# Kernel tuning notes

Measured on AMD Instinct MI355X. Metric: run time of the kernel, lower is better.

The kernel has to match this reference:

```python
import jax, jax.numpy as jnp
import numpy as np

N_NODES = 16384
N_EDGES = 196608
N_ELEM = 8
C = 32              # hidden channels per l-block
LMAX = 3
SH_DIM = 16         # (LMAX+1)^2
NUM_BESSEL = 8
R_MAX = 5.0
P_CUT = 5.0
H_RAD = 64
AVG_NEIGH = 12.0
N_LAYERS = 2
L_SLICES = ((0, 1), (1, 4), (4, 9), (9, 16))  # l = 0..3 blocks


def real_sph_harm(u):
    # u: [E,3] unit vectors -> real spherical harmonics up to l=3, component-normalized. [E,16]
    x, y, z = u[:, 0], u[:, 1], u[:, 2]
    x2, y2, z2 = x * x, y * y, z * z
    sh = [
        jnp.ones_like(x),
        jnp.sqrt(3.) * x, jnp.sqrt(3.) * y, jnp.sqrt(3.) * z,
        jnp.sqrt(15.) * x * y, jnp.sqrt(15.) * y * z,
        jnp.sqrt(5.) / 2. * (3. * z2 - 1.), jnp.sqrt(15.) * x * z,
        jnp.sqrt(15.) / 2. * (x2 - y2),
        jnp.sqrt(35. / 8.) * y * (3. * x2 - y2), jnp.sqrt(105.) * x * y * z,
        jnp.sqrt(21. / 8.) * y * (5. * z2 - 1.), jnp.sqrt(7.) / 2. * z * (5. * z2 - 3.),
        jnp.sqrt(21. / 8.) * x * (5. * z2 - 1.), jnp.sqrt(105.) / 2. * z * (x2 - y2),
        jnp.sqrt(35. / 8.) * x * (x2 - 3. * y2),
    ]
    return jnp.stack(sh, axis=-1)


def bessel_cutoff(r):
    # Bessel radial basis * polynomial cutoff (MACE radial embedding). r: [E] -> [E, NUM_BESSEL]
    u = r / R_MAX
    n = jnp.arange(1, NUM_BESSEL + 1, dtype=r.dtype)
    safe_r = jnp.maximum(r, 1e-9)
    rb = jnp.sqrt(2.0 / R_MAX) * jnp.sin(jnp.pi * n * u[:, None]) / safe_r[:, None]
    p = P_CUT
    fc = 1.0 - (p + 1.) * (p + 2.) / 2. * u ** p + p * (p + 2.) * u ** (p + 1.) - p * (p + 1.) / 2. * u ** (p + 2.)
    fc = fc * (u < 1.0).astype(r.dtype)
    return rb * fc[:, None]


def per_l_linear(a, W):
    # equivariant per-l channel mixing. a: [N,C,16], W: [4,C,C]
    outs = [jnp.einsum('nci,co->noi', a[:, :, s:e], W[l]) for l, (s, e) in enumerate(L_SLICES)]
    return jnp.concatenate(outs, axis=-1)


def mace_descriptors(atom_pos, node_attrs, shifts, edge_index,
                     W_embed, W1, W2, W3, W4, Wlin, Wskip, w2, w3, Wprod):
    snd, rcv = edge_index[0], edge_index[1]
    vec = atom_pos[rcv] - atom_pos[snd] + shifts            # [E,3]
    length = jnp.sqrt(jnp.sum(vec * vec, axis=-1) + 1e-18)  # [E]
    unit = vec / length[:, None]
    edge_attrs = real_sph_harm(unit)                        # [E,16]
    edge_feats = bessel_cutoff(length)                      # [E,8]

    node_scal = node_attrs @ W_embed                        # [N,C] node embedding (l=0)
    node_feats = jnp.zeros((atom_pos.shape[0], C, SH_DIM), dtype=atom_pos.dtype).at[:, :, 0].set(node_scal)

    descs = []
    for i in range(N_LAYERS):
        # radial MLP -> per-edge tensor-product weights
        h = jax.nn.silu(edge_feats @ W1[i])
        h = jax.nn.silu(h @ W2[i])
        h = jax.nn.silu(h @ W3[i])
        tpw = (h @ W4[i]).reshape(-1, C, SH_DIM)            # [E,C,16]
        # gather -> channelwise tensor product with edge spherical harmonics
        s = node_feats[:, :, 0][snd]                        # [E,C] invariant sender feats
        msg = tpw * edge_attrs[:, None, :] * s[:, :, None]  # [E,C,16]
        # scatter-add aggregation
        agg = jax.ops.segment_sum(msg.reshape(-1, C * SH_DIM), rcv,
                                  num_segments=N_NODES) / AVG_NEIGH
        a = per_l_linear(agg.reshape(-1, C, SH_DIM), Wlin[i])
        # element-dependent residual (skip tensor product with one-hot node attrs)
        sc = jnp.einsum('nz,ncm,zco->nom', node_attrs, node_feats, Wskip[i])
        # symmetric-contraction-style product block (correlation up to 3, invariants)
        inv = a[:, :, 0]
        p2 = jnp.sum(a * a, axis=-1)                        # power-spectrum invariant [N,C]
        b0 = inv + w2[i] * p2 + w3[i] * inv * p2
        b = a.at[:, :, 0].set(b0)
        node_feats = per_l_linear(b, Wprod[i]) + sc
        descs.append(node_feats[:, :, 0])                   # invariant slice
    return jnp.concatenate(descs, axis=-1)                  # [N, N_LAYERS*C]


def setup_inputs() -> dict:
    key = jax.random.key(0)
    ks = jax.random.split(key, 16)
    atom_pos = jax.random.normal(ks[0], (N_NODES, 3), dtype=jnp.float32) * 1.8
    elem = jax.random.randint(ks[1], (N_NODES,), 0, N_ELEM)
    node_attrs = jax.nn.one_hot(elem, N_ELEM, dtype=jnp.float32)
    shifts = jnp.zeros((N_EDGES, 3), dtype=jnp.float32)
    edge_index = jax.random.randint(ks[2], (2, N_EDGES), 0, N_NODES)
    f32 = jnp.float32
    W_embed = jax.random.normal(ks[3], (N_ELEM, C), f32) / np.sqrt(N_ELEM)
    W1 = jax.random.normal(ks[4], (N_LAYERS, NUM_BESSEL, H_RAD), f32) / np.sqrt(NUM_BESSEL)
    W2 = jax.random.normal(ks[5], (N_LAYERS, H_RAD, H_RAD), f32) / np.sqrt(H_RAD)
    W3 = jax.random.normal(ks[6], (N_LAYERS, H_RAD, H_RAD), f32) / np.sqrt(H_RAD)
    W4 = jax.random.normal(ks[7], (N_LAYERS, H_RAD, C * SH_DIM), f32) / np.sqrt(H_RAD)
    Wlin = jax.random.normal(ks[8], (N_LAYERS, 4, C, C), f32) / np.sqrt(C)
    Wskip = jax.random.normal(ks[9], (N_LAYERS, N_ELEM, C, C), f32) / np.sqrt(N_ELEM * C)
    w2 = jax.random.normal(ks[10], (N_LAYERS, C), f32) * 0.1
    w3 = jax.random.normal(ks[11], (N_LAYERS, C), f32) * 0.1
    Wprod = jax.random.normal(ks[12], (N_LAYERS, 4, C, C), f32) / np.sqrt(C)
    return {"atom_pos": atom_pos, "node_attrs": node_attrs, "shifts": shifts,
            "edge_index": edge_index, "W_embed": W_embed, "W1": W1, "W2": W2,
            "W3": W3, "W4": W4, "Wlin": Wlin, "Wskip": Wskip, "w2": w2,
            "w3": w3, "Wprod": Wprod}


def reference(atom_pos, node_attrs, shifts, edge_index, W_embed, W1, W2, W3, W4,
              Wlin, Wskip, w2, w3, Wprod):
    return mace_descriptors(atom_pos, node_attrs, shifts, edge_index,
                            W_embed, W1, W2, W3, W4, Wlin, Wskip, w2, w3, Wprod)
```

## Files before the change

### kernel.cpp

```cpp
#include <hip/hip_runtime.h>
#include <math.h>

#define N_NODES_C 16384
#define N_EDGES_C 196608

typedef short bf16x8 __attribute__((ext_vector_type(8)));
typedef float f32x4 __attribute__((ext_vector_type(4)));
typedef float f32x8 __attribute__((ext_vector_type(8)));

__device__ __forceinline__ float silu_f(float x) {
  return x * __builtin_amdgcn_rcpf(1.0f + __expf(-x));
}

__global__ void k_count(const int* __restrict__ rcv, int* __restrict__ counts) {
  int e = blockIdx.x * 256 + threadIdx.x;
  atomicAdd(&counts[rcv[e]], 1);
}

__global__ __launch_bounds__(1024) void k_scan(const int* __restrict__ counts,
                                               int* __restrict__ row_start,
                                               int* __restrict__ cursor) {
  __shared__ int sums[1024];
  const int tid = threadIdx.x;
  int loc[16];
  int s = 0;
#pragma unroll
  for (int i = 0; i < 16; ++i) { loc[i] = counts[tid * 16 + i]; s += loc[i]; }
  sums[tid] = s;
  __syncthreads();
  for (int off = 1; off < 1024; off <<= 1) {
    int t = (tid >= off) ? sums[tid - off] : 0;
    __syncthreads();
    sums[tid] += t;
    __syncthreads();
  }
  int excl = sums[tid] - s;
#pragma unroll
  for (int i = 0; i < 16; ++i) {
    row_start[tid * 16 + i] = excl;
    cursor[tid * 16 + i] = excl;
    excl += loc[i];
  }
  if (tid == 1023) row_start[N_NODES_C] = excl;
}

__global__ void k_fill(const int* __restrict__ rcv, int* __restrict__ cursor,
                       int* __restrict__ elist) {
  int e = blockIdx.x * 256 + threadIdx.x;
  int slot = atomicAdd(&cursor[rcv[e]], 1);
  elist[slot] = e;
}

__global__ void k_elem(const float* __restrict__ attrs, int* __restrict__ elem) {
  int n = blockIdx.x * 256 + threadIdx.x;
  const float* a = attrs + n * 8;
  int best = 0;
  float bv = a[0];
#pragma unroll
  for (int z = 1; z < 8; ++z) {
    if (a[z] > bv) { bv = a[z]; best = z; }
  }
  elem[n] = best;
}

__global__ void k_embed(const float* __restrict__ attrs, const float* __restrict__ Wemb,
                        float* __restrict__ scal0, float* __restrict__ nf) {
  int gid = blockIdx.x * 256 + threadIdx.x;
  int n = gid >> 5, c = gid & 31;
  float s = 0.f;
#pragma unroll
  for (int z = 0; z < 8; ++z) s = fmaf(attrs[n * 8 + z], Wemb[z * 32 + c], s);
  scal0[gid] = s;
  float* row = nf + (size_t)n * 512 + c * 16;
  *(float4*)&row[0] = make_float4(s, 0.f, 0.f, 0.f);
  *(float4*)&row[4] = make_float4(0.f, 0.f, 0.f, 0.f);
  *(float4*)&row[8] = make_float4(0.f, 0.f, 0.f, 0.f);
  *(float4*)&row[12] = make_float4(0.f, 0.f, 0.f, 0.f);
}

__global__ __launch_bounds__(256, 3) void k_radial(
    const float* __restrict__ pos, const float* __restrict__ shifts,
    const int* __restrict__ snd, const int* __restrict__ rcv,
    const int* __restrict__ elist, const float* __restrict__ scal,
    const float* __restrict__ W1g, const float* __restrict__ W2g,
    const float* __restrict__ W3g, unsigned short* __restrict__ h3,
    float* __restrict__ sedge, float* __restrict__ Yout, const int writeY) {
  __shared__ __align__(16) float efs[4][32][8];
  __shared__ __align__(16) float hbs[4][2][64];
  const int wid = threadIdx.x >> 6, lane = threadIdx.x & 63;
  float w1c[8], w2c[64], w3c[64];
#pragma unroll
  for (int k = 0; k < 8; ++k) w1c[k] = W1g[k * 64 + lane];
#pragma unroll
  for (int k = 0; k < 64; ++k) w2c[k] = W2g[k * 64 + lane];
#pragma unroll
  for (int k = 0; k < 64; ++k) w3c[k] = W3g[k * 64 + lane];

  const int base = (blockIdx.x * 4 + wid) * 32;

  if (lane < 32) {
    const int p = base + lane;
    const int e = elist[p];
    const int sn = snd[e], rc = rcv[e];
    const float vx = pos[rc * 3 + 0] - pos[sn * 3 + 0] + shifts[e * 3 + 0];
    const float vy = pos[rc * 3 + 1] - pos[sn * 3 + 1] + shifts[e * 3 + 1];
    const float vz = pos[rc * 3 + 2] - pos[sn * 3 + 2] + shifts[e * 3 + 2];
    const float len = __builtin_amdgcn_sqrtf(vx * vx + vy * vy + vz * vz + 1e-18f);
    const float u = len * 0.2f;
    float fc = 0.f;
    if (u < 1.0f) {
      const float u2 = u * u, u5 = u2 * u2 * u;
      fc = 1.0f - 21.0f * u5 + 35.0f * u5 * u - 15.0f * u5 * u2;
    }
    const float pref = 0.6324555320336759f * fc * __builtin_amdgcn_rcpf(fmaxf(len, 1e-9f));
    float efv[8];
#pragma unroll
    for (int k = 0; k < 8; ++k) {
      const float pin = 3.14159274f * (float)(k + 1);
      efv[k] = pref * __sinf(pin * u);
    }
    *(float4*)&efs[wid][lane][0] = make_float4(efv[0], efv[1], efv[2], efv[3]);
    *(float4*)&efs[wid][lane][4] = make_float4(efv[4], efv[5], efv[6], efv[7]);

    if (writeY) {
      const float il = __builtin_amdgcn_rcpf(len);
      const float x = vx * il, y = vy * il, z = vz * il;
      const float x2 = x * x, y2 = y * y, z2 = z * z;
      const float s3 = 1.7320508075688772f;
      const float s15 = 3.872983346207417f;
      const float s5h = 1.118033988749895f;
      const float s35_8 = 2.091650066335189f;
      const float s105 = 10.246950765959598f;
      const float s21_8 = 1.6201851746019651f;
      const float s7h = 1.3228756555322954f;
      const float s105h = 5.123475382979799f;
      float* yp = Yout + (size_t)p * 16;
      *(float4*)&yp[0] = make_float4(1.f, s3 * x, s3 * y, s3 * z);
      *(float4*)&yp[4] = make_float4(s15 * x * y, s15 * y * z, s5h * (3.f * z2 - 1.f), s15 * x * z);
      *(float4*)&yp[8] = make_float4(0.5f * s15 * (x2 - y2), s35_8 * y * (3.f * x2 - y2),
                                     s105 * x * y * z, s21_8 * y * (5.f * z2 - 1.f));
      *(float4*)&yp[12] = make_float4(s7h * z * (5.f * z2 - 3.f), s21_8 * x * (5.f * z2 - 1.f),
                                      s105h * z * (x2 - y2), s35_8 * x * (x2 - 3.f * y2));
    }
  }

  {
    const int p2 = base + (lane >> 1);
    const int e2 = elist[p2];
    const int sn2 = snd[e2];
    const int co = (lane & 1) * 16;
    const float* sp = scal + (size_t)sn2 * 32 + co;
    float* dp = sedge + (size_t)p2 * 32 + co;
    *(float4*)&dp[0] = *(const float4*)&sp[0];
    *(float4*)&dp[4] = *(const float4*)&sp[4];
    *(float4*)&dp[8] = *(const float4*)&sp[8];
    *(float4*)&dp[12] = *(const float4*)&sp[12];
  }

  for (int t = 0; t < 16; ++t) {
    const float4 eA0 = *(const float4*)&efs[wid][t][0];
    const float4 eA1 = *(const float4*)&efs[wid][t][4];
    const float4 eB0 = *(const float4*)&efs[wid][t + 16][0];
    const float4 eB1 = *(const float4*)&efs[wid][t + 16][4];
    float aA = eA0.x * w1c[0], aB = eB0.x * w1c[0];
    aA = fmaf(eA0.y, w1c[1], aA); aB = fmaf(eB0.y, w1c[1], aB);
    aA = fmaf(eA0.z, w1c[2], aA); aB = fmaf(eB0.z, w1c[2], aB);
    aA = fmaf(eA0.w, w1c[3], aA); aB = fmaf(eB0.w, w1c[3], aB);
    aA = fmaf(eA1.x, w1c[4], aA); aB = fmaf(eB1.x, w1c[4], aB);
    aA = fmaf(eA1.y, w1c[5], aA); aB = fmaf(eB1.y, w1c[5], aB);
    aA = fmaf(eA1.z, w1c[6], aA); aB = fmaf(eB1.z, w1c[6], aB);
    aA = fmaf(eA1.w, w1c[7], aA); aB = fmaf(eB1.w, w1c[7], aB);
    hbs[wid][0][lane] = silu_f(aA);
    hbs[wid][1][lane] = silu_f(aB);
    float pA0 = 0.f, pA1 = 0.f, pA2 = 0.f, pA3 = 0.f;
    float pB0 = 0.f, pB1 = 0.f, pB2 = 0.f, pB3 = 0.f;
#pragma unroll
    for (int k4 = 0; k4 < 16; ++k4) {
      const float4 hA = *(const float4*)&hbs[wid][0][k4 * 4];
      const float4 hB = *(const float4*)&hbs[wid][1][k4 * 4];
      pA0 = fmaf(hA.x, w2c[k4 * 4 + 0], pA0); pB0 = fmaf(hB.x, w2c[k4 * 4 + 0], pB0);
      pA1 = fmaf(hA.y, w2c[k4 * 4 + 1], pA1); pB1 = fmaf(hB.y, w2c[k4 * 4 + 1], pB1);
      pA2 = fmaf(hA.z, w2c[k4 * 4 + 2], pA2); pB2 = fmaf(hB.z, w2c[k4 * 4 + 2], pB2);
      pA3 = fmaf(hA.w, w2c[k4 * 4 + 3], pA3); pB3 = fmaf(hB.w, w2c[k4 * 4 + 3], pB3);
    }
    hbs[wid][0][lane] = silu_f((pA0 + pA1) + (pA2 + pA3));
    hbs[wid][1][lane] = silu_f((pB0 + pB1) + (pB2 + pB3));
    pA0 = pA1 = pA2 = pA3 = 0.f;
    pB0 = pB1 = pB2 = pB3 = 0.f;
#pragma unroll
    for (int k4 = 0; k4 < 16; ++k4) {
      const float4 hA = *(const float4*)&hbs[wid][0][k4 * 4];
      const float4 hB = *(const float4*)&hbs[wid][1][k4 * 4];
      pA0 = fmaf(hA.x, w3c[k4 * 4 + 0], pA0); pB0 = fmaf(hB.x, w3c[k4 * 4 + 0], pB0);
      pA1 = fmaf(hA.y, w3c[k4 * 4 + 1], pA1); pB1 = fmaf(hB.y, w3c[k4 * 4 + 1], pB1);
      pA2 = fmaf(hA.z, w3c[k4 * 4 + 2], pA2); pB2 = fmaf(hB.z, w3c[k4 * 4 + 2], pB2);
      pA3 = fmaf(hA.w, w3c[k4 * 4 + 3], pA3); pB3 = fmaf(hB.w, w3c[k4 * 4 + 3], pB3);
    }
    const float hvA = silu_f((pA0 + pA1) + (pA2 + pA3));
    const float hvB = silu_f((pB0 + pB1) + (pB2 + pB3));
    const unsigned hbA = __float_as_uint(hvA) & 0xFFFF0000u;
    const unsigned hbB = __float_as_uint(hvB) & 0xFFFF0000u;
    const float loA = hvA - __uint_as_float(hbA);
    const float loB = hvB - __uint_as_float(hbB);
    h3[(size_t)(base + t) * 128 + lane] = (unsigned short)(hbA >> 16);
    h3[(size_t)(base + t) * 128 + 64 + lane] = (unsigned short)(__float_as_uint(loA) >> 16);
    h3[(size_t)(base + 16 + t) * 128 + lane] = (unsigned short)(hbB >> 16);
    h3[(size_t)(base + 16 + t) * 128 + 64 + lane] = (unsigned short)(__float_as_uint(loB) >> 16);
  }
}

__global__ __launch_bounds__(256, 4) void k_gather(
    const unsigned short* __restrict__ h3, const float* __restrict__ W4g,
    const float* __restrict__ Yb, const float* __restrict__ sedge,
    const int* __restrict__ row_start, float* __restrict__ agg) {
  __shared__ __align__(16) short blo_lds[4][4][2][64][8];
  const int ch = (blockIdx.x >> 3) & 1;
  const int ng = ((blockIdx.x >> 4) << 3) | (blockIdx.x & 7);
  const int w = threadIdx.x >> 6, lane = threadIdx.x & 63;
  const int grp = lane >> 4, lm = lane & 15;

  bf16x8 bhi[4][2];
#pragma unroll
  for (int t = 0; t < 4; ++t) {
    const int col = ch * 256 + w * 64 + t * 16 + lm;
#pragma unroll
    for (int kk = 0; kk < 2; ++kk) {
      bf16x8 lo;
#pragma unroll
      for (int j = 0; j < 8; ++j) {
        const float wv = W4g[(kk * 32 + grp * 8 + j) * 512 + col];
        const unsigned hb = __float_as_uint(wv) & 0xFFFF0000u;
        bhi[t][kk][j] = (short)(hb >> 16);
        lo[j] = (short)(__float_as_uint(wv - __uint_as_float(hb)) >> 16);
      }
      *(bf16x8*)&blo_lds[w][t][kk][lane][0] = lo;
    }
  }
  __syncthreads();

  const int nBeg = ng * 8;
  for (int n = nBeg; n < nBeg + 8; ++n) {
    const int e0 = row_start[n], e1 = row_start[n + 1];
    float outv[4] = {0.f, 0.f, 0.f, 0.f};
    for (int p0 = e0; p0 < e1; p0 += 16) {
      bf16x8 ahi0 = {0, 0, 0, 0, 0, 0, 0, 0}, ahi1 = ahi0, alo0 = ahi0, alo1 = ahi0;
      const int pa = p0 + lm;
      if (pa < e1) {
        const unsigned short* hp = h3 + (size_t)pa * 128 + grp * 8;
        ahi0 = *(const bf16x8*)(hp);
        ahi1 = *(const bf16x8*)(hp + 32);
        alo0 = *(const bf16x8*)(hp + 64);
        alo1 = *(const bf16x8*)(hp + 96);
      }
      float ys[4][4];
#pragma unroll
      for (int r = 0; r < 4; ++r) {
        const int pr = p0 + grp * 4 + r;
        const float Yv = Yb[(size_t)pr * 16 + lm];
        const float4 s4 = *(const float4*)&sedge[(size_t)pr * 32 + ch * 16 + w * 4];
        ys[r][0] = Yv * s4.x;
        ys[r][1] = Yv * s4.y;
        ys[r][2] = Yv * s4.z;
        ys[r][3] = Yv * s4.w;
      }
#pragma unroll
      for (int t = 0; t < 4; ++t) {
        f32x4 acc = {0.f, 0.f, 0.f, 0.f};
        acc = __builtin_amdgcn_mfma_f32_16x16x32_bf16(ahi0, bhi[t][0], acc, 0, 0, 0);
        acc = __builtin_amdgcn_mfma_f32_16x16x32_bf16(ahi1, bhi[t][1], acc, 0, 0, 0);
        acc = __builtin_amdgcn_mfma_f32_16x16x32_bf16(alo0, bhi[t][0], acc, 0, 0, 0);
        acc = __builtin_amdgcn_mfma_f32_16x16x32_bf16(alo1, bhi[t][1], acc, 0, 0, 0);
        const bf16x8 bl0 = *(const bf16x8*)&blo_lds[w][t][0][lane][0];
        const bf16x8 bl1 = *(const bf16x8*)&blo_lds[w][t][1][lane][0];
        acc = __builtin_amdgcn_mfma_f32_16x16x32_bf16(ahi0, bl0, acc, 0, 0, 0);
        acc = __builtin_amdgcn_mfma_f32_16x16x32_bf16(ahi1, bl1, acc, 0, 0, 0);
        float cp = acc[0] * ys[0][t];
        cp = fmaf(acc[1], ys[1][t], cp);
        cp = fmaf(acc[2], ys[2][t], cp);
        cp = fmaf(acc[3], ys[3][t], cp);
        outv[t] += cp;
      }
    }
    const float inv12 = 1.0f / 12.0f;
#pragma unroll
    for (int t = 0; t < 4; ++t) {
      outv[t] += __shfl_xor(outv[t], 16);
      outv[t] += __shfl_xor(outv[t], 32);
      if (grp == t)
        agg[(size_t)n * 512 + ch * 256 + w * 64 + t * 16 + lm] = outv[t] * inv12;
    }
  }
}

__global__ __launch_bounds__(256) void k_node(
    const float* __restrict__ agg, float* __restrict__ nf,
    const float* __restrict__ Wlin, const float* __restrict__ Wprod,
    const float* __restrict__ Wskip, const float* __restrict__ w2v,
    const float* __restrict__ w3v, const int* __restrict__ elem,
    float* __restrict__ scal_out, float* __restrict__ dout, const int layer) {
  __shared__ __align__(16) float aggs[8][512];
  __shared__ __align__(16) float nfs[8][512];
  __shared__ float bs[8][544];
  const int tid = threadIdx.x;
  const int n0 = blockIdx.x * 8;
  for (int i = tid; i < 1024; i += 256) {
    const int nl = i >> 7, qq = i & 127;
    ((f32x4*)aggs)[i] = ((const f32x4*)agg)[(size_t)(n0 + nl) * 128 + qq];
    ((f32x4*)nfs)[i] = ((const f32x4*)nf)[(size_t)(n0 + nl) * 128 + qq];
  }
  __syncthreads();
  const int nl = tid >> 5, o = tid & 31;
  const int n = n0 + nl;
  constexpr int SLa[4] = {0, 1, 4, 9};
  constexpr int ELa[4] = {1, 4, 9, 16};
  float a[16];
#pragma unroll
  for (int m = 0; m < 16; ++m) a[m] = 0.f;
#pragma unroll
  for (int l = 0; l < 4; ++l) {
    for (int c = 0; c < 32; ++c) {
      const float w = Wlin[(l * 32 + c) * 32 + o];
#pragma unroll
      for (int m = SLa[l]; m < ELa[l]; ++m) a[m] = fmaf(aggs[nl][c * 16 + m], w, a[m]);
    }
  }
  const float inv = a[0];
  float p2 = 0.f;
#pragma unroll
  for (int m = 0; m < 16; ++m) p2 = fmaf(a[m], a[m], p2);
  a[0] = inv + w2v[o] * p2 + w3v[o] * inv * p2;
#pragma unroll
  for (int m = 0; m < 16; ++m) bs[nl][o * 17 + m] = a[m];
  __syncthreads();
  float outv[16];
#pragma unroll
  for (int m = 0; m < 16; ++m) outv[m] = 0.f;
#pragma unroll
  for (int l = 0; l < 4; ++l) {
    for (int c = 0; c < 32; ++c) {
      const float w = Wprod[(l * 32 + c) * 32 + o];
#pragma unroll
      for (int m = SLa[l]; m < ELa[l]; ++m) outv[m] = fmaf(bs[nl][c * 17 + m], w, outv[m]);
    }
  }
  const int z = elem[n];
  const float* wsk = Wskip + z * 1024;
  for (int c = 0; c < 32; ++c) {
    const float w = wsk[c * 32 + o];
#pragma unroll
    for (int m = 0; m < 16; ++m) outv[m] = fmaf(nfs[nl][c * 16 + m], w, outv[m]);
  }
  float* op = nf + (size_t)n * 512 + o * 16;
  *(float4*)&op[0] = make_float4(outv[0], outv[1], outv[2], outv[3]);
  *(float4*)&op[4] = make_float4(outv[4], outv[5], outv[6], outv[7]);
  *(float4*)&op[8] = make_float4(outv[8], outv[9], outv[10], outv[11]);
  *(float4*)&op[12] = make_float4(outv[12], outv[13], outv[14], outv[15]);
  scal_out[n * 32 + o] = outv[0];
  dout[(size_t)n * 64 + layer * 32 + o] = outv[0];
}

extern "C" void kernel_launch(void* const* d_in, const int* in_sizes, int n_in,
                              void* d_out, int out_size, void* d_ws, size_t ws_size,
                              hipStream_t stream) {
  const float* pos = (const float*)d_in[0];
  const float* attrs = (const float*)d_in[1];
  const float* shifts = (const float*)d_in[2];
  const int* eidx = (const int*)d_in[3];
  const float* W_embed = (const float*)d_in[4];
  const float* W1 = (const float*)d_in[5];
  const float* W2 = (const float*)d_in[6];
  const float* W3 = (const float*)d_in[7];
  const float* W4 = (const float*)d_in[8];
  const float* Wlin = (const float*)d_in[9];
  const float* Wskip = (const float*)d_in[10];
  const float* w2v = (const float*)d_in[11];
  const float* w3v = (const float*)d_in[12];
  const float* Wprod = (const float*)d_in[13];
  float* out = (float*)d_out;
  const int* snd = eidx;
  const int* rcv = eidx + N_EDGES_C;

  char* p = (char*)d_ws;
  auto take = [&](size_t bytes) {
    char* q = p;
    p += (bytes + 255) & ~(size_t)255;
    return q;
  };
  int* counts = (int*)take((size_t)N_NODES_C * 4);
  int* row_start = (int*)take((size_t)(N_NODES_C + 1) * 4);
  int* cursor = (int*)take((size_t)N_NODES_C * 4);
  int* elist = (int*)take((size_t)N_EDGES_C * 4);
  int* elem = (int*)take((size_t)N_NODES_C * 4);
  float* Ybuf = (float*)take((size_t)(N_EDGES_C + 16) * 16 * 4);
  unsigned short* h3 = (unsigned short*)take((size_t)(N_EDGES_C + 16) * 128 * 2);
  float* sedge = (float*)take((size_t)(N_EDGES_C + 16) * 32 * 4);
  float* agg = (float*)take((size_t)N_NODES_C * 512 * 4);
  float* nf = (float*)take((size_t)N_NODES_C * 512 * 4);
  float* scal0 = (float*)take((size_t)N_NODES_C * 32 * 4);
  float* scal1 = (float*)take((size_t)N_NODES_C * 32 * 4);
  (void)ws_size; (void)in_sizes; (void)n_in; (void)out_size;

  hipMemsetAsync(counts, 0, (size_t)N_NODES_C * 4, stream);
  k_count<<<N_EDGES_C / 256, 256, 0, stream>>>(rcv, counts);
  k_scan<<<1, 1024, 0, stream>>>(counts, row_start, cursor);
  k_fill<<<N_EDGES_C / 256, 256, 0, stream>>>(rcv, cursor, elist);
  k_elem<<<N_NODES_C / 256, 256, 0, stream>>>(attrs, elem);
  k_embed<<<N_NODES_C * 32 / 256, 256, 0, stream>>>(attrs, W_embed, scal0, nf);

  for (int i = 0; i < 2; ++i) {
    k_radial<<<1536, 256, 0, stream>>>(pos, shifts, snd, rcv, elist,
                                       i == 0 ? scal0 : scal1,
                                       W1 + (size_t)i * 8 * 64, W2 + (size_t)i * 64 * 64,
                                       W3 + (size_t)i * 64 * 64, h3, sedge, Ybuf,
                                       i == 0 ? 1 : 0);
    k_gather<<<4096, 256, 0, stream>>>(h3, W4 + (size_t)i * 64 * 512, Ybuf, sedge,
                                       row_start, agg);
    k_node<<<N_NODES_C / 8, 256, 0, stream>>>(agg, nf, Wlin + (size_t)i * 4096,
                                              Wprod + (size_t)i * 4096,
                                              Wskip + (size_t)i * 8192,
                                              w2v + (size_t)i * 32, w3v + (size_t)i * 32,
                                              elem, scal1, out, i);
  }
}
```

Measured before the change: 535.8 us.

## Load-balance gather over 16-edge tiles with atomic accumulation for split nodes

Builds a per-node tile prefix scan and a tile descriptor list, so the gather kernel walks a flat, evenly chunked range of 16-edge tiles instead of looping over eight nodes per block. Nodes spanning more than one tile accumulate with atomics into an aggregation buffer that is zeroed first, and single-tile nodes write directly. The low-half W4 fragments move from LDS into registers, with occupancy lowered from 4 to 3 waves to make room. This adds a memset per layer, a tile-build kernel and some atomic traffic, and the MAX_TILES bound assumes the tile count stays under 32768.

```diff
diff --git a/kernel.cpp b/kernel.cpp
--- a/kernel.cpp
+++ b/kernel.cpp
@@ -3,6 +3,7 @@
 
 #define N_NODES_C 16384
 #define N_EDGES_C 196608
+#define MAX_TILES 32768
 
 typedef short bf16x8 __attribute__((ext_vector_type(8)));
 typedef float f32x4 __attribute__((ext_vector_type(4)));
@@ -19,29 +20,43 @@
 
 __global__ __launch_bounds__(1024) void k_scan(const int* __restrict__ counts,
                                                int* __restrict__ row_start,
-                                               int* __restrict__ cursor) {
-  __shared__ int sums[1024];
+                                               int* __restrict__ cursor,
+                                               int* __restrict__ tstart) {
+  __shared__ int s1a[1024];
+  __shared__ int s2a[1024];
   const int tid = threadIdx.x;
   int loc[16];
-  int s = 0;
-#pragma unroll
-  for (int i = 0; i < 16; ++i) { loc[i] = counts[tid * 16 + i]; s += loc[i]; }
-  sums[tid] = s;
+  int s1 = 0, s2 = 0;
+#pragma unroll
+  for (int i = 0; i < 16; ++i) {
+    loc[i] = counts[tid * 16 + i];
+    s1 += loc[i];
+    s2 += (loc[i] + 15) >> 4;
+  }
+  s1a[tid] = s1;
+  s2a[tid] = s2;
   __syncthreads();
   for (int off = 1; off < 1024; off <<= 1) {
-    int t = (tid >= off) ? sums[tid - off] : 0;
+    int t1 = (tid >= off) ? s1a[tid - off] : 0;
+    int t2 = (tid >= off) ? s2a[tid - off] : 0;
     __syncthreads();
-    sums[tid] += t;
+    s1a[tid] += t1;
+    s2a[tid] += t2;
     __syncthreads();
   }
-  int excl = sums[tid] - s;
+  int e1 = s1a[tid] - s1, e2 = s2a[tid] - s2;
 #pragma unroll
   for (int i = 0; i < 16; ++i) {
-    row_start[tid * 16 + i] = excl;
-    cursor[tid * 16 + i] = excl;
-    excl += loc[i];
-  }
-  if (tid == 1023) row_start[N_NODES_C] = excl;
+    row_start[tid * 16 + i] = e1;
+    cursor[tid * 16 + i] = e1;
+    tstart[tid * 16 + i] = e2;
+    e1 += loc[i];
+    e2 += (loc[i] + 15) >> 4;
+  }
+  if (tid == 1023) {
+    row_start[N_NODES_C] = e1;
+    tstart[N_NODES_C] = e2;
+  }
 }
 
 __global__ void k_fill(const int* __restrict__ rcv, int* __restrict__ cursor,
@@ -49,6 +64,21 @@
   int e = blockIdx.x * 256 + threadIdx.x;
   int slot = atomicAdd(&cursor[rcv[e]], 1);
   elist[slot] = e;
+}
+
+__global__ void k_tiles(const int* __restrict__ row_start, const int* __restrict__ tstart,
+                        int2* __restrict__ tdesc) {
+  const int n = blockIdx.x * 256 + threadIdx.x;
+  const int e0 = row_start[n], e1 = row_start[n + 1];
+  const int cnt = e1 - e0;
+  const int nt = (cnt + 15) >> 4;
+  const int t0 = tstart[n];
+  const unsigned mbit = (nt > 1) ? 0x80000000u : 0u;
+  for (int j = 0; j < nt; ++j) {
+    int len = cnt - 16 * j;
+    if (len > 16) len = 16;
+    tdesc[t0 + j] = make_int2((int)((unsigned)n | ((unsigned)len << 20) | mbit), e0 + 16 * j);
+  }
 }
 
 __global__ void k_elem(const float* __restrict__ attrs, int* __restrict__ elem) {
@@ -209,85 +239,96 @@
   }
 }
 
-__global__ __launch_bounds__(256, 4) void k_gather(
+__global__ __launch_bounds__(256, 3) void k_gather(
     const unsigned short* __restrict__ h3, const float* __restrict__ W4g,
     const float* __restrict__ Yb, const float* __restrict__ sedge,
-    const int* __restrict__ row_start, float* __restrict__ agg) {
-  __shared__ __align__(16) short blo_lds[4][4][2][64][8];
-  const int ch = (blockIdx.x >> 3) & 1;
-  const int ng = ((blockIdx.x >> 4) << 3) | (blockIdx.x & 7);
+    const int2* __restrict__ tdesc, const int* __restrict__ ntiles_ptr,
+    float* __restrict__ agg) {
+  const int bid = blockIdx.x;
+  const int xcd = bid & 7, q = bid >> 3, half = q & 1;
+  const int s = ((q >> 1) << 3) | xcd;
   const int w = threadIdx.x >> 6, lane = threadIdx.x & 63;
   const int grp = lane >> 4, lm = lane & 15;
-
-  bf16x8 bhi[4][2];
+  const int cg = half * 4 + w;
+
+  bf16x8 bhi[4][2], blo[4][2];
 #pragma unroll
   for (int t = 0; t < 4; ++t) {
-    const int col = ch * 256 + w * 64 + t * 16 + lm;
+    const int col = cg * 64 + t * 16 + lm;
 #pragma unroll
     for (int kk = 0; kk < 2; ++kk) {
-      bf16x8 lo;
 #pragma unroll
       for (int j = 0; j < 8; ++j) {
         const float wv = W4g[(kk * 32 + grp * 8 + j) * 512 + col];
         const unsigned hb = __float_as_uint(wv) & 0xFFFF0000u;
         bhi[t][kk][j] = (short)(hb >> 16);
-        lo[j] = (short)(__float_as_uint(wv - __uint_as_float(hb)) >> 16);
+        blo[t][kk][j] = (short)(__float_as_uint(wv - __uint_as_float(hb)) >> 16);
       }
-      *(bf16x8*)&blo_lds[w][t][kk][lane][0] = lo;
-    }
-  }
-  __syncthreads();
-
-  const int nBeg = ng * 8;
-  for (int n = nBeg; n < nBeg + 8; ++n) {
-    const int e0 = row_start[n], e1 = row_start[n + 1];
-    float outv[4] = {0.f, 0.f, 0.f, 0.f};
-    for (int p0 = e0; p0 < e1; p0 += 16) {
-      bf16x8 ahi0 = {0, 0, 0, 0, 0, 0, 0, 0}, ahi1 = ahi0, alo0 = ahi0, alo1 = ahi0;
-      const int pa = p0 + lm;
-      if (pa < e1) {
-        const unsigned short* hp = h3 + (size_t)pa * 128 + grp * 8;
-        ahi0 = *(const bf16x8*)(hp);
-        ahi1 = *(const bf16x8*)(hp + 32);
-        alo0 = *(const bf16x8*)(hp + 64);
-        alo1 = *(const bf16x8*)(hp + 96);
+    }
+  }
+
+  const int ntiles = *ntiles_ptr;
+  const int chunk = (ntiles + 1023) >> 10;
+  const int tbeg = s * chunk;
+  const float inv12 = 1.0f / 12.0f;
+
+  for (int j = 0; j < chunk; ++j) {
+    const int ti = tbeg + j;
+    if (ti >= ntiles) break;
+    const int2 td = tdesc[ti];
+    const unsigned x = (unsigned)td.x;
+    const int node = (int)(x & 0x3FFFu);
+    const int len = (int)((x >> 20) & 31u);
+    const bool multi = (x & 0x80000000u) != 0u;
+    const int p0 = td.y;
+
+    const unsigned short* hp = h3 + (size_t)(p0 + lm) * 128 + grp * 8;
+    const bf16x8 ahi0 = *(const bf16x8*)(hp);
+    const bf16x8 ahi1 = *(const bf16x8*)(hp + 32);
+    const bf16x8 alo0 = *(const bf16x8*)(hp + 64);
+    const bf16x8 alo1 = *(const bf16x8*)(hp + 96);
+
+    float ys[4][4];
+#pragma unroll
+    for (int r = 0; r < 4; ++r) {
+      const int rr = grp * 4 + r;
+      const int pr = p0 + rr;
+      const float yraw = Yb[(size_t)pr * 16 + lm];
+      const float Yv = (rr < len) ? yraw * inv12 : 0.f;
+      const float4 s4 = *(const float4*)&sedge[(size_t)pr * 32 + cg * 4];
+      ys[r][0] = Yv * s4.x;
+      ys[r][1] = Yv * s4.y;
+      ys[r][2] = Yv * s4.z;
+      ys[r][3] = Yv * s4.w;
+    }
+
+    float outv[4];
+#pragma unroll
+    for (int t = 0; t < 4; ++t) {
+      f32x4 acc = {0.f, 0.f, 0.f, 0.f};
+      acc = __builtin_amdgcn_mfma_f32_16x16x32_bf16(ahi0, bhi[t][0], acc, 0, 0, 0);
+      acc = __builtin_amdgcn_mfma_f32_16x16x32_bf16(ahi1, bhi[t][1], acc, 0, 0, 0);
+      acc = __builtin_amdgcn_mfma_f32_16x16x32_bf16(alo0, bhi[t][0], acc, 0, 0, 0);
+      acc = __builtin_amdgcn_mfma_f32_16x16x32_bf16(alo1, bhi[t][1], acc, 0, 0, 0);
+      acc = __builtin_amdgcn_mfma_f32_16x16x32_bf16(ahi0, blo[t][0], acc, 0, 0, 0);
+      acc = __builtin_amdgcn_mfma_f32_16x16x32_bf16(ahi1, blo[t][1], acc, 0, 0, 0);
+      float cp = acc[0] * ys[0][t];
+      cp = fmaf(acc[1], ys[1][t], cp);
+      cp = fmaf(acc[2], ys[2][t], cp);
+      cp = fmaf(acc[3], ys[3][t], cp);
+      cp += __shfl_xor(cp, 16);
+      cp += __shfl_xor(cp, 32);
+      outv[t] = cp;
+    }
+#pragma unroll
+    for (int t = 0; t < 4; ++t) {
+      if (grp == t) {
+        float* ap = &agg[(size_t)node * 512 + cg * 64 + t * 16 + lm];
+        if (multi)
+          atomicAdd(ap, outv[t]);
+        else
+          *ap = outv[t];
       }
-      float ys[4][4];
-#pragma unroll
-      for (int r = 0; r < 4; ++r) {
-        const int pr = p0 + grp * 4 + r;
-        const float Yv = Yb[(size_t)pr * 16 + lm];
-        const float4 s4 = *(const float4*)&sedge[(size_t)pr * 32 + ch * 16 + w * 4];
-        ys[r][0] = Yv * s4.x;
-        ys[r][1] = Yv * s4.y;
-        ys[r][2] = Yv * s4.z;
-        ys[r][3] = Yv * s4.w;
-      }
-#pragma unroll
-      for (int t = 0; t < 4; ++t) {
-        f32x4 acc = {0.f, 0.f, 0.f, 0.f};
-        acc = __builtin_amdgcn_mfma_f32_16x16x32_bf16(ahi0, bhi[t][0], acc, 0, 0, 0);
-        acc = __builtin_amdgcn_mfma_f32_16x16x32_bf16(ahi1, bhi[t][1], acc, 0, 0, 0);
-        acc = __builtin_amdgcn_mfma_f32_16x16x32_bf16(alo0, bhi[t][0], acc, 0, 0, 0);
-        acc = __builtin_amdgcn_mfma_f32_16x16x32_bf16(alo1, bhi[t][1], acc, 0, 0, 0);
-        const bf16x8 bl0 = *(const bf16x8*)&blo_lds[w][t][0][lane][0];
-        const bf16x8 bl1 = *(const bf16x8*)&blo_lds[w][t][1][lane][0];
-        acc = __builtin_amdgcn_mfma_f32_16x16x32_bf16(ahi0, bl0, acc, 0, 0, 0);
-        acc = __builtin_amdgcn_mfma_f32_16x16x32_bf16(ahi1, bl1, acc, 0, 0, 0);
-        float cp = acc[0] * ys[0][t];
-        cp = fmaf(acc[1], ys[1][t], cp);
-        cp = fmaf(acc[2], ys[2][t], cp);
-        cp = fmaf(acc[3], ys[3][t], cp);
-        outv[t] += cp;
-      }
-    }
-    const float inv12 = 1.0f / 12.0f;
-#pragma unroll
-    for (int t = 0; t < 4; ++t) {
-      outv[t] += __shfl_xor(outv[t], 16);
-      outv[t] += __shfl_xor(outv[t], 32);
-      if (grp == t)
-        agg[(size_t)n * 512 + ch * 256 + w * 64 + t * 16 + lm] = outv[t] * inv12;
     }
   }
 }
@@ -389,7 +430,9 @@
   int* counts = (int*)take((size_t)N_NODES_C * 4);
   int* row_start = (int*)take((size_t)(N_NODES_C + 1) * 4);
   int* cursor = (int*)take((size_t)N_NODES_C * 4);
+  int* tstart = (int*)take((size_t)(N_NODES_C + 1) * 4);
   int* elist = (int*)take((size_t)N_EDGES_C * 4);
+  int2* tdesc = (int2*)take((size_t)MAX_TILES * 8);
   int* elem = (int*)take((size_t)N_NODES_C * 4);
   float* Ybuf = (float*)take((size_t)(N_EDGES_C + 16) * 16 * 4);
   unsigned short* h3 = (unsigned short*)take((size_t)(N_EDGES_C + 16) * 128 * 2);
@@ -402,8 +445,9 @@
 
   hipMemsetAsync(counts, 0, (size_t)N_NODES_C * 4, stream);
   k_count<<<N_EDGES_C / 256, 256, 0, stream>>>(rcv, counts);
-  k_scan<<<1, 1024, 0, stream>>>(counts, row_start, cursor);
+  k_scan<<<1, 1024, 0, stream>>>(counts, row_start, cursor, tstart);
   k_fill<<<N_EDGES_C / 256, 256, 0, stream>>>(rcv, cursor, elist);
+  k_tiles<<<N_NODES_C / 256, 256, 0, stream>>>(row_start, tstart, tdesc);
   k_elem<<<N_NODES_C / 256, 256, 0, stream>>>(attrs, elem);
   k_embed<<<N_NODES_C * 32 / 256, 256, 0, stream>>>(attrs, W_embed, scal0, nf);
 
@@ -413,8 +457,9 @@
                                        W1 + (size_t)i * 8 * 64, W2 + (size_t)i * 64 * 64,
                                        W3 + (size_t)i * 64 * 64, h3, sedge, Ybuf,
                                        i == 0 ? 1 : 0);
-    k_gather<<<4096, 256, 0, stream>>>(h3, W4 + (size_t)i * 64 * 512, Ybuf, sedge,
-                                       row_start, agg);
+    hipMemsetAsync(agg, 0, (size_t)N_NODES_C * 512 * 4, stream);
+    k_gather<<<2048, 256, 0, stream>>>(h3, W4 + (size_t)i * 64 * 512, Ybuf, sedge,
+                                       tdesc, tstart + N_NODES_C, agg);
     k_node<<<N_NODES_C / 8, 256, 0, stream>>>(agg, nf, Wlin + (size_t)i * 4096,
                                               Wprod + (size_t)i * 4096,
                                               Wskip + (size_t)i * 8192,
```

Measured after the change: 568.1 us. +6.0%, slower.
